# Performance work log

Hardware: AMD Instinct MI355X
Metric: run time of the kernel (lower is better)

Reference implementation:

```python
import jax, jax.numpy as jnp
import numpy as np


def _unit(h):
    # F.normalize(p=2, dim=-1) equivalent (NormalizeFunc 'unit')
    n = jnp.sqrt(jnp.sum(h * h, axis=-1, keepdims=True))
    return h / jnp.maximum(n, 1e-12)


def setup_inputs() -> dict:
    key = jax.random.key(0)
    k = jax.random.split(key, 6)
    B, T, D, size = 48, 32, 1024, 512
    x = jax.random.normal(k[0], (B, T, D), dtype=jnp.float32)
    w_leaf = jax.random.normal(k[1], (D, size), dtype=jnp.float32) / np.sqrt(D)
    b_leaf = jnp.zeros((size,), dtype=jnp.float32)
    w_comp = jax.random.normal(k[2], (2 * size, size), dtype=jnp.float32) / np.sqrt(2 * size)
    b_comp = jnp.zeros((size,), dtype=jnp.float32)
    s_bilinear = jax.random.normal(k[3], (size, size), dtype=jnp.float32) / np.sqrt(size)
    return {"x": x, "w_leaf": w_leaf, "b_leaf": b_leaf,
            "w_comp": w_comp, "b_comp": b_comp, "s_bilinear": s_bilinear}


def reference(x, w_leaf, b_leaf, w_comp, b_comp, s_bilinear):
    B, T, D = x.shape
    size = w_leaf.shape[1]
    # chart offsets: level lv occupies offsets[lv] : offsets[lv] + (T - lv)
    offsets = np.concatenate([[0], np.cumsum(T - np.arange(T))]).astype(np.int64)
    ncells = T * (T + 1) // 2

    # leaf_transform: MLP + unit normalization
    leaf = _unit(jax.nn.relu(x @ w_leaf + b_leaf))  # [B, T, size]
    chart_h = jnp.zeros((B, ncells, size), x.dtype).at[:, :T].set(leaf)
    chart_s = jnp.zeros((B, ncells, 1), x.dtype)

    for level in range(1, T):
        L = T - level  # spans at this level
        N = level      # split points per span
        pos = np.arange(L)[:, None]
        n = np.arange(N)[None, :]
        # left child: level n at pos; right child: level (level-n-1) at pos+n+1
        l_idx = offsets[n] + pos                       # [L, N]
        r_idx = offsets[level - n - 1] + pos + n + 1   # [L, N]

        lh = chart_h[:, l_idx]  # [B, L, N, size]
        rh = chart_h[:, r_idx]  # [B, L, N, size]
        ls = chart_s[:, l_idx]  # [B, L, N, 1]
        rs = chart_s[:, r_idx]  # [B, L, N, 1]

        # inside_compose: MLP over concatenated children
        h = jax.nn.relu(jnp.concatenate([lh, rh], axis=-1) @ w_comp + b_comp)
        # inside_score: bilinear compatibility
        xs = jnp.einsum('blnd,de,blne->bln', lh, s_bilinear, rh)[..., None]
        s = xs + ls + rs                  # [B, L, N, 1]
        p = jax.nn.softmax(s, axis=2)
        hbar = _unit(jnp.sum(h * p, axis=2))  # [B, L, size]
        sbar = jnp.sum(s * p, axis=2)         # [B, L, 1]

        off = int(offsets[level])
        chart_h = chart_h.at[:, off:off + L].set(hbar)
        chart_s = chart_s.at[:, off:off + L].set(sbar)

    return chart_h
```

## Files before the change

### kernel.cpp

```cpp
#include <hip/hip_runtime.h>
#include <math.h>

#define BB 48
#define TT 32
#define DD 1024
#define SZ 512
#define NCELLS 528

typedef unsigned short u16;
typedef unsigned int u32;
typedef __attribute__((ext_vector_type(8))) short bf16x8;
typedef __attribute__((ext_vector_type(4))) float f32x4;

__device__ __forceinline__ int off_of(int k) { return TT * k - (k * (k - 1)) / 2; }

__device__ __forceinline__ u16 f2bf(float x) {
    u32 u = __float_as_uint(x);
    u32 r = (u + 0x7fffu + ((u >> 16) & 1u)) >> 16;
    return (u16)r;
}
__device__ __forceinline__ float bf2f(u16 h) {
    return __uint_as_float(((u32)h) << 16);
}
__device__ __forceinline__ u32 pack2(u16 a, u16 b) {
    return (u32)a | ((u32)b << 16);
}
__device__ __forceinline__ float2 upk(u32 v) {
    return make_float2(__uint_as_float(v << 16),
                       __uint_as_float(v & 0xffff0000u));
}

__global__ __launch_bounds__(256) void prep_w(
    const float* __restrict__ w_comp, const float* __restrict__ s_bil,
    u16* __restrict__ WT)
{
    int idx = blockIdx.x * 256 + threadIdx.x;
    int n = idx >> 9, k = idx & 511;
    float w;
    if (n < 512)       w = w_comp[(size_t)k * SZ + n];
    else if (n < 1024) w = w_comp[(size_t)(512 + k) * SZ + (n - 512)];
    else               w = s_bil[(size_t)k * SZ + (n - 1024)];
    WT[idx] = f2bf(w);
}

__global__ __launch_bounds__(256) void prep_wl(
    const float* __restrict__ w_leaf,
    u16* __restrict__ WLT_hi, u16* __restrict__ WLT_lo)
{
    int idx = blockIdx.x * 256 + threadIdx.x;
    int n = idx >> 10, k = idx & 1023;
    float w = w_leaf[(size_t)k * SZ + n];
    u16 hi = f2bf(w);
    u16 lo = f2bf(w - bf2f(hi));
    WLT_hi[idx] = hi;
    WLT_lo[idx] = lo;
}

__global__ __launch_bounds__(256) void leaf_mfma(
    const float* __restrict__ x,
    const u16* __restrict__ WLT_hi, const u16* __restrict__ WLT_lo,
    const float* __restrict__ b_leaf, float* __restrict__ leaf_pre)
{
    __shared__ u16 Ah[128][40];
    __shared__ u16 Bh[64][40], Bl[64][40];

    const int col0 = blockIdx.x * 64;
    const int row0 = blockIdx.y * 128;
    const int t = threadIdx.x;

    const int srow = t >> 1, skh = (t & 1) * 16;
    const float* ap = x + (size_t)(row0 + srow) * DD + skh;
    const int bcol = t >> 2, bch = (t & 3) * 8;
    const u16* bph = WLT_hi + (size_t)(col0 + bcol) * DD + bch;
    const u16* bpl = WLT_lo + (size_t)(col0 + bcol) * DD + bch;

    const int lane = t & 63, wv = t >> 6;
    const int wr = wv >> 1, wc = wv & 1;
    const int l15 = lane & 15, lko = (lane >> 4) * 8;

    f32x4 acc[4][2];
    #pragma unroll
    for (int i = 0; i < 4; ++i)
        #pragma unroll
        for (int j = 0; j < 2; ++j)
            #pragma unroll
            for (int e = 0; e < 4; ++e) acc[i][j][e] = 0.f;

    float4 pa[4];
    uint4 pbh, pbl;
    #pragma unroll
    for (int c = 0; c < 4; ++c) pa[c] = *(const float4*)(ap + c * 4);
    pbh = *(const uint4*)bph;
    pbl = *(const uint4*)bpl;

    for (int k0 = 0; k0 < DD; k0 += 32) {
        u32 wh[8];
        #pragma unroll
        for (int c = 0; c < 4; ++c) {
            wh[c * 2]     = pack2(f2bf(pa[c].x), f2bf(pa[c].y));
            wh[c * 2 + 1] = pack2(f2bf(pa[c].z), f2bf(pa[c].w));
        }
        *(uint4*)&Ah[srow][skh]     = make_uint4(wh[0], wh[1], wh[2], wh[3]);
        *(uint4*)&Ah[srow][skh + 8] = make_uint4(wh[4], wh[5], wh[6], wh[7]);
        *(uint4*)&Bh[bcol][bch] = pbh;
        *(uint4*)&Bl[bcol][bch] = pbl;
        __syncthreads();

        if (k0 + 32 < DD) {
            #pragma unroll
            for (int c = 0; c < 4; ++c)
                pa[c] = *(const float4*)(ap + k0 + 32 + c * 4);
            pbh = *(const uint4*)(bph + k0 + 32);
            pbl = *(const uint4*)(bpl + k0 + 32);
        }

        bf16x8 fah[4], fbh[2], fbl[2];
        #pragma unroll
        for (int i = 0; i < 4; ++i)
            fah[i] = *(const bf16x8*)&Ah[wr * 64 + i * 16 + l15][lko];
        #pragma unroll
        for (int j = 0; j < 2; ++j) {
            fbh[j] = *(const bf16x8*)&Bh[wc * 32 + j * 16 + l15][lko];
            fbl[j] = *(const bf16x8*)&Bl[wc * 32 + j * 16 + l15][lko];
        }
        #pragma unroll
        for (int i = 0; i < 4; ++i) {
            #pragma unroll
            for (int j = 0; j < 2; ++j) {
                acc[i][j] = __builtin_amdgcn_mfma_f32_16x16x32_bf16(
                    fah[i], fbh[j], acc[i][j], 0, 0, 0);
                acc[i][j] = __builtin_amdgcn_mfma_f32_16x16x32_bf16(
                    fah[i], fbl[j], acc[i][j], 0, 0, 0);
            }
        }
        __syncthreads();
    }

    #pragma unroll
    for (int i = 0; i < 4; ++i) {
        int rbase = row0 + wr * 64 + i * 16 + (lane >> 4) * 4;
        #pragma unroll
        for (int j = 0; j < 2; ++j) {
            int gc = col0 + wc * 32 + j * 16 + l15;
            float bc = b_leaf[gc];
            #pragma unroll
            for (int q = 0; q < 4; ++q)
                leaf_pre[(size_t)(rbase + q) * SZ + gc] =
                    fmaxf(acc[i][j][q] + bc, 0.f);
        }
    }
}

__global__ __launch_bounds__(256) void leaf_norm(
    const float* __restrict__ leaf_pre, float* __restrict__ chart_h,
    u16* __restrict__ Hchart, float* __restrict__ Sarr)
{
    const int r = blockIdx.x;
    const int b = r >> 5, pos = r & 31;
    const int cell = b * NCELLS + pos;
    const int t = threadIdx.x, lane = t & 63, wave = t >> 6;
    __shared__ float red[4];

    float2 v = *(const float2*)&leaf_pre[(size_t)r * SZ + 2 * t];
    float sq = v.x * v.x + v.y * v.y;
    #pragma unroll
    for (int o = 32; o; o >>= 1) sq += __shfl_xor(sq, o);
    if (lane == 0) red[wave] = sq;
    __syncthreads();
    float nrm = sqrtf(red[0] + red[1] + red[2] + red[3]);
    float inv = 1.f / fmaxf(nrm, 1e-12f);
    v.x *= inv; v.y *= inv;
    *(float2*)&chart_h[(size_t)cell * SZ + 2 * t] = v;
    ((u32*)Hchart)[(size_t)cell * 256 + t] = pack2(f2bf(v.x), f2bf(v.y));
    if (t == 0) Sarr[cell] = 0.f;
}

__global__ __launch_bounds__(256) void transform_mfma(
    const u16* __restrict__ Hchart, const u16* __restrict__ WT,
    const float* __restrict__ b_comp,
    u16* __restrict__ ACU, int level, int nrt)
{
    __shared__ u16 Ah[64][40];
    __shared__ u16 Bh[64][40];
    __shared__ int cidx[64];

    const int L = TT - level, rows = BB * L, off = off_of(level);
    const int id = blockIdx.x;
    const int w = (id & 7) * (3 * nrt) + (id >> 3);
    const int ct = w / nrt, rt = w % nrt;
    const int col0 = ct * 64;

    const int t = threadIdx.x;
    if (t < 64) {
        int g = rt * 64 + t;
        cidx[t] = (g < rows) ? ((g / L) * NCELLS + off + (g % L)) : -1;
    }

    const int srow = t >> 2, skc = (t & 3) * 8;
    int ga = rt * 64 + srow;
    if (ga >= rows) ga = rows - 1;
    const int acell = (ga / L) * NCELLS + off + (ga % L);
    const u16* aph = Hchart + (size_t)acell * SZ + skc;
    const u16* bph = WT + (size_t)(col0 + srow) * SZ + skc;

    const int lane = t & 63, wv = t >> 6;
    const int wr = wv >> 1, wc = wv & 1;
    const int l15 = lane & 15, lko = (lane >> 4) * 8;

    f32x4 acc[2][2];
    #pragma unroll
    for (int i = 0; i < 2; ++i)
        #pragma unroll
        for (int j = 0; j < 2; ++j)
            #pragma unroll
            for (int e = 0; e < 4; ++e) acc[i][j][e] = 0.f;

    uint4 pah = *(const uint4*)aph;
    uint4 pbh = *(const uint4*)bph;

    for (int k0 = 0; k0 < SZ; k0 += 32) {
        *(uint4*)&Ah[srow][skc] = pah;
        *(uint4*)&Bh[srow][skc] = pbh;
        __syncthreads();

        if (k0 + 32 < SZ) {
            pah = *(const uint4*)(aph + k0 + 32);
            pbh = *(const uint4*)(bph + k0 + 32);
        }

        bf16x8 fah[2], fbh[2];
        #pragma unroll
        for (int i = 0; i < 2; ++i)
            fah[i] = *(const bf16x8*)&Ah[wr * 32 + i * 16 + l15][lko];
        #pragma unroll
        for (int j = 0; j < 2; ++j)
            fbh[j] = *(const bf16x8*)&Bh[wc * 32 + j * 16 + l15][lko];
        #pragma unroll
        for (int i = 0; i < 2; ++i)
            #pragma unroll
            for (int j = 0; j < 2; ++j)
                acc[i][j] = __builtin_amdgcn_mfma_f32_16x16x32_bf16(
                    fah[i], fbh[j], acc[i][j], 0, 0, 0);
        __syncthreads();
    }

    #pragma unroll
    for (int i = 0; i < 2; ++i) {
        int rbase = wr * 32 + i * 16 + (lane >> 4) * 4;
        #pragma unroll
        for (int j = 0; j < 2; ++j) {
            int gc = col0 + wc * 32 + j * 16 + l15;
            float bias = (gc < 512) ? b_comp[gc] : 0.f;
            #pragma unroll
            for (int q = 0; q < 4; ++q) {
                int ci = cidx[rbase + q];
                if (ci >= 0)
                    ACU[(size_t)ci * 1536 + gc] = f2bf(acc[i][j][q] + bias);
            }
        }
    }
}

__global__ __launch_bounds__(256) void combine_kernel(
    float* __restrict__ chart_h, const u16* __restrict__ ACU,
    const u16* __restrict__ Hchart,
    float* __restrict__ Sarr, u16* __restrict__ Hchart_w, int level)
{
    const int L = TT - level, N = level;
    const int b = blockIdx.x / L, pos = blockIdx.x % L;
    const int off = off_of(level);

    __shared__ float s_lds[32], p_lds[32];
    __shared__ int lcell[32], rcell[32];
    __shared__ float hred[4][512];
    __shared__ float red[4];

    const int t = threadIdx.x, lane = t & 63, wv = t >> 6;

    if (t < N) {
        lcell[t] = b * NCELLS + off_of(t) + pos;
        rcell[t] = b * NCELLS + off_of(level - t - 1) + pos + t + 1;
    }
    __syncthreads();

    for (int n = wv; n < N; n += 4) {
        const u16* u  = ACU + (size_t)lcell[n] * 1536 + 1024;
        const u16* hr = Hchart + (size_t)rcell[n] * SZ;
        uint4 uv = *(const uint4*)&u[lane * 8];
        uint4 hv = *(const uint4*)&hr[lane * 8];
        float d = 0.f;
        {
            float2 a = upk(uv.x), h2 = upk(hv.x);
            d = fmaf(a.x, h2.x, fmaf(a.y, h2.y, d));
        }
        {
            float2 a = upk(uv.y), h2 = upk(hv.y);
            d = fmaf(a.x, h2.x, fmaf(a.y, h2.y, d));
        }
        {
            float2 a = upk(uv.z), h2 = upk(hv.z);
            d = fmaf(a.x, h2.x, fmaf(a.y, h2.y, d));
        }
        {
            float2 a = upk(uv.w), h2 = upk(hv.w);
            d = fmaf(a.x, h2.x, fmaf(a.y, h2.y, d));
        }
        #pragma unroll
        for (int o = 32; o; o >>= 1) d += __shfl_xor(d, o);
        if (lane == 0)
            s_lds[n] = d + Sarr[lcell[n]] + Sarr[rcell[n]];
    }
    __syncthreads();

    if (wv == 0) {
        float sv = (lane < N) ? s_lds[lane] : -INFINITY;
        float m = sv;
        #pragma unroll
        for (int o = 32; o; o >>= 1) m = fmaxf(m, __shfl_xor(m, o));
        float e = (lane < N) ? expf(sv - m) : 0.f;
        float sum = e;
        #pragma unroll
        for (int o = 32; o; o >>= 1) sum += __shfl_xor(sum, o);
        float p = e / sum;
        if (lane < N) p_lds[lane] = p;
        float sb = (lane < N) ? sv * p : 0.f;
        #pragma unroll
        for (int o = 32; o; o >>= 1) sb += __shfl_xor(sb, o);
        if (lane == 0) Sarr[(size_t)b * NCELLS + off + pos] = sb;
    }
    __syncthreads();

    float hacc[8];
    #pragma unroll
    for (int q = 0; q < 8; ++q) hacc[q] = 0.f;
    for (int n = wv; n < N; n += 4) {
        const u16* A_ = ACU + (size_t)lcell[n] * 1536;
        const u16* C_ = ACU + (size_t)rcell[n] * 1536 + 512;
        uint4 va = *(const uint4*)&A_[lane * 8];
        uint4 vc = *(const uint4*)&C_[lane * 8];
        float p = p_lds[n];
        const u32 av[4] = {va.x, va.y, va.z, va.w};
        const u32 cv[4] = {vc.x, vc.y, vc.z, vc.w};
        #pragma unroll
        for (int c = 0; c < 4; ++c) {
            float2 a2 = upk(av[c]);
            float2 c2 = upk(cv[c]);
            hacc[c * 2]     = fmaf(p, fmaxf(a2.x + c2.x, 0.f), hacc[c * 2]);
            hacc[c * 2 + 1] = fmaf(p, fmaxf(a2.y + c2.y, 0.f), hacc[c * 2 + 1]);
        }
    }
    *(float4*)&hred[wv][lane * 8]     = *(float4*)&hacc[0];
    *(float4*)&hred[wv][lane * 8 + 4] = *(float4*)&hacc[4];
    __syncthreads();

    float hx = hred[0][2 * t] + hred[1][2 * t] + hred[2][2 * t] + hred[3][2 * t];
    float hy = hred[0][2 * t + 1] + hred[1][2 * t + 1]
             + hred[2][2 * t + 1] + hred[3][2 * t + 1];

    float sq = hx * hx + hy * hy;
    #pragma unroll
    for (int o = 32; o; o >>= 1) sq += __shfl_xor(sq, o);
    if (lane == 0) red[wv] = sq;
    __syncthreads();
    float nrm = sqrtf(red[0] + red[1] + red[2] + red[3]);
    float inv = 1.f / fmaxf(nrm, 1e-12f);
    hx *= inv; hy *= inv;
    const int ocell = b * NCELLS + off + pos;
    *(float2*)&chart_h[(size_t)ocell * SZ + 2 * t] = make_float2(hx, hy);
    ((u32*)Hchart_w)[(size_t)ocell * 256 + t] = pack2(f2bf(hx), f2bf(hy));
}

extern "C" void kernel_launch(void* const* d_in, const int* in_sizes, int n_in,
                              void* d_out, int out_size, void* d_ws, size_t ws_size,
                              hipStream_t stream)
{
    const float* x      = (const float*)d_in[0];
    const float* w_leaf = (const float*)d_in[1];
    const float* b_leaf = (const float*)d_in[2];
    const float* w_comp = (const float*)d_in[3];
    const float* b_comp = (const float*)d_in[4];
    const float* s_bil  = (const float*)d_in[5];
    float* chart_h = (float*)d_out;

    char* ws = (char*)d_ws;
    u16* ACU    = (u16*)ws;                        ws += (size_t)BB * NCELLS * 1536 * 2;
    u16* Hchart = (u16*)ws;                        ws += (size_t)BB * NCELLS * SZ * 2;
    float* Sarr = (float*)ws;                      ws += (size_t)BB * NCELLS * 4;
    u16* WT     = (u16*)ws;                        ws += (size_t)1536 * SZ * 2;
    u16* WLT_hi = (u16*)ws;                        ws += (size_t)SZ * DD * 2;
    u16* WLT_lo = (u16*)ws;                        ws += (size_t)SZ * DD * 2;
    float* leaf_pre = (float*)ws;                  ws += (size_t)BB * TT * SZ * 4;

    prep_w<<<(1536 * SZ) / 256, 256, 0, stream>>>(w_comp, s_bil, WT);
    prep_wl<<<(SZ * DD) / 256, 256, 0, stream>>>(w_leaf, WLT_hi, WLT_lo);
    leaf_mfma<<<dim3(8, 12), 256, 0, stream>>>(x, WLT_hi, WLT_lo, b_leaf, leaf_pre);
    leaf_norm<<<BB * TT, 256, 0, stream>>>(leaf_pre, chart_h, Hchart, Sarr);

    {
        int nrt = (BB * TT + 63) / 64;
        transform_mfma<<<24 * nrt, 256, 0, stream>>>(
            Hchart, WT, b_comp, ACU, 0, nrt);
    }

    for (int level = 1; level < TT; ++level) {
        int L = TT - level;
        combine_kernel<<<BB * L, 256, 0, stream>>>(
            chart_h, ACU, Hchart, Sarr, Hchart, level);
        if (level < TT - 1) {
            int nrt = (BB * L + 63) / 64;
            transform_mfma<<<24 * nrt, 256, 0, stream>>>(
                Hchart, WT, b_comp, ACU, level, nrt);
        }
    }
}
```

Measured before the change: 654.7 us.

## Widen combine kernel to 512 threads and swizzle block order across XCDs

The combine kernel now launches 8 waves per block instead of 4, so each wave handles fewer split points and the per-block reduction over splits uses 8 partial buffers. Block indices are remapped so consecutive blocks spread across 8 groups, which likely targets XCD-aware L2 locality on the multi-die GPU. The span-score prefix loads (Sarr for the left and right cells) are hoisted into the cell-index setup. In exchange, LDS use doubles, an extra barrier is added for the final store, and half the threads sit idle during the output write.

After: 636.5 us. -2.8%, faster.

```diff
diff --git a/kernel.cpp b/kernel.cpp
--- a/kernel.cpp
+++ b/kernel.cpp
@@ -261,29 +261,34 @@
     }
 }
 
-__global__ __launch_bounds__(256) void combine_kernel(
+__global__ __launch_bounds__(512) void combine_kernel(
     float* __restrict__ chart_h, const u16* __restrict__ ACU,
     const u16* __restrict__ Hchart,
     float* __restrict__ Sarr, u16* __restrict__ Hchart_w, int level)
 {
     const int L = TT - level, N = level;
-    const int b = blockIdx.x / L, pos = blockIdx.x % L;
+    const int cpx = (BB * L) >> 3;
+    const int swz = (blockIdx.x & 7) * cpx + (blockIdx.x >> 3);
+    const int b = swz / L, pos = swz % L;
     const int off = off_of(level);
 
-    __shared__ float s_lds[32], p_lds[32];
+    __shared__ float s_lds[32], p_lds[32], spre[32];
     __shared__ int lcell[32], rcell[32];
-    __shared__ float hred[4][512];
-    __shared__ float red[4];
+    __shared__ float hred[8][512];
+    __shared__ float red[8];
 
     const int t = threadIdx.x, lane = t & 63, wv = t >> 6;
 
     if (t < N) {
-        lcell[t] = b * NCELLS + off_of(t) + pos;
-        rcell[t] = b * NCELLS + off_of(level - t - 1) + pos + t + 1;
-    }
-    __syncthreads();
-
-    for (int n = wv; n < N; n += 4) {
+        int lc = b * NCELLS + off_of(t) + pos;
+        int rc = b * NCELLS + off_of(level - t - 1) + pos + t + 1;
+        lcell[t] = lc;
+        rcell[t] = rc;
+        spre[t] = Sarr[lc] + Sarr[rc];
+    }
+    __syncthreads();
+
+    for (int n = wv; n < N; n += 8) {
         const u16* u  = ACU + (size_t)lcell[n] * 1536 + 1024;
         const u16* hr = Hchart + (size_t)rcell[n] * SZ;
         uint4 uv = *(const uint4*)&u[lane * 8];
@@ -307,8 +312,7 @@
         }
         #pragma unroll
         for (int o = 32; o; o >>= 1) d += __shfl_xor(d, o);
-        if (lane == 0)
-            s_lds[n] = d + Sarr[lcell[n]] + Sarr[rcell[n]];
+        if (lane == 0) s_lds[n] = d + spre[n];
     }
     __syncthreads();
 
@@ -333,7 +337,7 @@
     float hacc[8];
     #pragma unroll
     for (int q = 0; q < 8; ++q) hacc[q] = 0.f;
-    for (int n = wv; n < N; n += 4) {
+    for (int n = wv; n < N; n += 8) {
         const u16* A_ = ACU + (size_t)lcell[n] * 1536;
         const u16* C_ = ACU + (size_t)rcell[n] * 1536 + 512;
         uint4 va = *(const uint4*)&A_[lane * 8];
@@ -353,21 +357,26 @@
     *(float4*)&hred[wv][lane * 8 + 4] = *(float4*)&hacc[4];
     __syncthreads();
 
-    float hx = hred[0][2 * t] + hred[1][2 * t] + hred[2][2 * t] + hred[3][2 * t];
-    float hy = hred[0][2 * t + 1] + hred[1][2 * t + 1]
-             + hred[2][2 * t + 1] + hred[3][2 * t + 1];
-
-    float sq = hx * hx + hy * hy;
+    float hv = hred[0][t] + hred[1][t] + hred[2][t] + hred[3][t]
+             + hred[4][t] + hred[5][t] + hred[6][t] + hred[7][t];
+
+    float sq = hv * hv;
     #pragma unroll
     for (int o = 32; o; o >>= 1) sq += __shfl_xor(sq, o);
     if (lane == 0) red[wv] = sq;
     __syncthreads();
-    float nrm = sqrtf(red[0] + red[1] + red[2] + red[3]);
+    float nrm = sqrtf(((red[0] + red[1]) + (red[2] + red[3]))
+                    + ((red[4] + red[5]) + (red[6] + red[7])));
     float inv = 1.f / fmaxf(nrm, 1e-12f);
-    hx *= inv; hy *= inv;
+    hv *= inv;
+    hred[0][t] = hv;
+    __syncthreads();
     const int ocell = b * NCELLS + off + pos;
-    *(float2*)&chart_h[(size_t)ocell * SZ + 2 * t] = make_float2(hx, hy);
-    ((u32*)Hchart_w)[(size_t)ocell * 256 + t] = pack2(f2bf(hx), f2bf(hy));
+    if (t < 256) {
+        float x0 = hred[0][2 * t], x1 = hred[0][2 * t + 1];
+        *(float2*)&chart_h[(size_t)ocell * SZ + 2 * t] = make_float2(x0, x1);
+        ((u32*)Hchart_w)[(size_t)ocell * 256 + t] = pack2(f2bf(x0), f2bf(x1));
+    }
 }
 
 extern "C" void kernel_launch(void* const* d_in, const int* in_sizes, int n_in,
@@ -404,7 +413,7 @@
 
     for (int level = 1; level < TT; ++level) {
         int L = TT - level;
-        combine_kernel<<<BB * L, 256, 0, stream>>>(
+        combine_kernel<<<BB * L, 512, 0, stream>>>(
             chart_h, ACU, Hchart, Sarr, Hchart, level);
         if (level < TT - 1) {
             int nrt = (BB * L + 63) / 64;
```
